# Kernel optimization log

Hardware: AMD Instinct MI355X
Metric: run time of the kernel (lower is better)

## Reference

```python
import jax, jax.numpy as jnp
import numpy as np
from jax import lax

EPS = 1e-6

def _instance_norm(x):
    # torch: std over flattened spatial, unbiased (ddof=1), + 1e-6
    b, c = x.shape[:2]
    xf = x.reshape(b, c, -1)
    mean = xf.mean(axis=2)[:, :, None, None]
    std = (jnp.std(xf, axis=2, ddof=1) + EPS)[:, :, None, None]
    return (x - mean) / std

def _conv1x1(x, w, b):
    # w: [O, I], x: [B, I, H, W]
    return jnp.einsum('oi,bihw->bohw', w, x) + b[None, :, None, None]

def _adaattn(content, style, ckey, skey, fw, fb, gw, gb, hw, hb):
    F = _conv1x1(ckey, fw, fb)   # [b, Ck, hc, wc]
    G = _conv1x1(skey, gw, gb)   # [b, Ck, hs, ws]
    H = _conv1x1(style, hw, hb)  # [b, Cv, hs, ws]
    b_, Ck, hc, wc = F.shape
    hs, ws = G.shape[2], G.shape[3]
    Fq = F.reshape(b_, Ck, hc * wc).transpose(0, 2, 1)   # [b, Nc, Ck]
    Gk = G.reshape(b_, Ck, hs * ws)                      # [b, Ck, Ns]
    Vs = H.reshape(b_, -1, hs * ws).transpose(0, 2, 1)   # [b, Ns, Cv]
    # Ns == hs*ws <= max_sample (4096) for these shapes -> no subsampling branch
    S = jax.nn.softmax(jnp.einsum('bnc,bcm->bnm', Fq, Gk), axis=-1)  # [b, Nc, Ns]
    mean = jnp.einsum('bnm,bmv->bnv', S, Vs)              # attention-weighted mean
    ex2 = jnp.einsum('bnm,bmv->bnv', S, Vs * Vs)          # E[x^2]
    std = jnp.sqrt(jax.nn.relu(ex2 - mean * mean))        # sqrt(relu(E[x^2]-E[x]^2))
    mean = mean.reshape(b_, hc, wc, -1).transpose(0, 3, 1, 2)
    std = std.reshape(b_, hc, wc, -1).transpose(0, 3, 1, 2)
    return std * _instance_norm(content) + mean

def _upsample2(x):
    return jnp.repeat(jnp.repeat(x, 2, axis=2), 2, axis=3)

def _conv3x3_reflect(x, w, b):
    xp = jnp.pad(x, ((0, 0), (0, 0), (1, 1), (1, 1)), mode='reflect')
    y = lax.conv_general_dilated(xp, w, window_strides=(1, 1), padding='VALID',
                                 dimension_numbers=('NCHW', 'OIHW', 'NCHW'))
    return y + b[None, :, None, None]


def setup_inputs() -> dict:
    key = jax.random.key(0)
    ks = jax.random.split(key, 16)
    f32 = jnp.float32
    d = {}
    d['content4_1'] = jax.random.normal(ks[0], (1, 512, 128, 128), f32)
    d['style4_1'] = jax.random.normal(ks[1], (1, 512, 64, 64), f32)
    d['content5_1'] = jax.random.normal(ks[2], (1, 512, 64, 64), f32)
    d['style5_1'] = jax.random.normal(ks[3], (1, 512, 32, 32), f32)
    d['content4_1_key'] = jax.random.normal(ks[4], (1, 960, 128, 128), f32)
    d['style4_1_key'] = jax.random.normal(ks[5], (1, 960, 64, 64), f32)
    d['content5_1_key'] = jax.random.normal(ks[6], (1, 1472, 64, 64), f32)
    d['style5_1_key'] = jax.random.normal(ks[7], (1, 1472, 32, 32), f32)
    def w2(k, o, i):
        return jax.random.normal(k, (o, i), f32) / np.sqrt(i).astype(np.float32)
    d['f4_w'] = w2(ks[8], 960, 960); d['f4_b'] = jnp.zeros((960,), f32)
    d['g4_w'] = w2(ks[9], 960, 960); d['g4_b'] = jnp.zeros((960,), f32)
    d['h4_w'] = w2(ks[10], 512, 512); d['h4_b'] = jnp.zeros((512,), f32)
    d['f5_w'] = w2(ks[11], 1472, 1472); d['f5_b'] = jnp.zeros((1472,), f32)
    d['g5_w'] = w2(ks[12], 1472, 1472); d['g5_b'] = jnp.zeros((1472,), f32)
    d['h5_w'] = w2(ks[13], 512, 512); d['h5_b'] = jnp.zeros((512,), f32)
    d['conv_w'] = jax.random.normal(ks[14], (512, 512, 3, 3), f32) / np.sqrt(512 * 9).astype(np.float32)
    d['conv_b'] = jnp.zeros((512,), f32)
    return d


def reference(content4_1, style4_1, content5_1, style5_1,
              content4_1_key, style4_1_key, content5_1_key, style5_1_key,
              f4_w, f4_b, g4_w, g4_b, h4_w, h4_b,
              f5_w, f5_b, g5_w, g5_b, h5_w, h5_b,
              conv_w, conv_b):
    a4 = _adaattn(content4_1, style4_1, content4_1_key, style4_1_key,
                  f4_w, f4_b, g4_w, g4_b, h4_w, h4_b)
    a5 = _adaattn(content5_1, style5_1, content5_1_key, style5_1_key,
                  f5_w, f5_b, g5_w, g5_b, h5_w, h5_b)
    return _conv3x3_reflect(a4 + _upsample2(a5), conv_w, conv_b)
```

## Files before the change

kernel.cpp:

```cpp
#include <hip/hip_runtime.h>
#include <math.h>


typedef _Float16 half8 __attribute__((ext_vector_type(8)));
typedef float f32x4 __attribute__((ext_vector_type(4)));

__device__ __forceinline__ void async16(const void* g, void* lds) {
    __builtin_amdgcn_global_load_lds(
        (const __attribute__((address_space(1))) void*)g,
        (__attribute__((address_space(3))) void*)lds, 16, 0, 0);
}

__device__ inline float wave_sum64(float v) {
#pragma unroll
    for (int o = 32; o > 0; o >>= 1) v += __shfl_xor(v, o, 64);
    return v;
}

template <int OUT>
__global__ __launch_bounds__(256, 2) void mgemm_hl(
    const _Float16* __restrict__ Ahi, const _Float16* __restrict__ Alo,
    const _Float16* __restrict__ Bhi, const _Float16* __restrict__ Blo,
    float* __restrict__ Cf, _Float16* __restrict__ Chi,
    _Float16* __restrict__ Clo, int K, int lda, int ldb, int ldc) {
    __shared__ _Float16 Ash[2][4096], Asl[2][4096], Bsh[2][4096], Bsl[2][4096];
    const int t = threadIdx.x, wave = t >> 6, lane = t & 63;
    const int bm = blockIdx.y * 128, bn = blockIdx.x * 128;
    const int wr = (wave >> 1) * 64, wc = (wave & 1) * 64;
    const int lq = lane >> 4, lr = lane & 15;
    const int srow = wave * 32 + (lane >> 2);
    const int scolg = (lane & 3) ^ ((lane >> 3) & 3);

    f32x4 acc[4][4] = {};

    const size_t aoff = (size_t)(bm + srow) * lda * 2 + scolg * 16;
    const size_t boff = (size_t)(bn + srow) * ldb * 2 + scolg * 16;
    const char* pAh = (const char*)Ahi + aoff;
    const char* pAl = (const char*)Alo + aoff;
    const char* pBh = (const char*)Bhi + boff;
    const char* pBl = (const char*)Blo + boff;
    const size_t ar = (size_t)16 * lda * 2, br = (size_t)16 * ldb * 2;
    const int dst = wave * 1024;
    const int key = (lr >> 1) & 3;

    auto stage = [&](int buf) {
        async16(pAh, &Ash[buf][dst]);
        async16(pAh + ar, &Ash[buf][dst + 512]);
        async16(pAl, &Asl[buf][dst]);
        async16(pAl + ar, &Asl[buf][dst + 512]);
        async16(pBh, &Bsh[buf][dst]);
        async16(pBh + br, &Bsh[buf][dst + 512]);
        async16(pBl, &Bsl[buf][dst]);
        async16(pBl + br, &Bsl[buf][dst + 512]);
        pAh += 64;
        pAl += 64;
        pBh += 64;
        pBl += 64;
    };

    const int NT = K >> 5;
    stage(0);
    for (int tt = 0; tt < NT; tt++) {
        __syncthreads();
        if (tt + 1 < NT) stage((tt + 1) & 1);
        const int cb = tt & 1;

        half8 ah[4], al[4], bh[4], bl[4];
#pragma unroll
        for (int i = 0; i < 4; i++) {
            const int ro = (wr + i * 16 + lr) * 32 + ((lq ^ key) * 8);
            ah[i] = *(const half8*)&Ash[cb][ro];
            al[i] = *(const half8*)&Asl[cb][ro];
        }
#pragma unroll
        for (int j = 0; j < 4; j++) {
            const int ro = (wc + j * 16 + lr) * 32 + ((lq ^ key) * 8);
            bh[j] = *(const half8*)&Bsh[cb][ro];
            bl[j] = *(const half8*)&Bsl[cb][ro];
        }
#pragma unroll
        for (int i = 0; i < 4; i++)
#pragma unroll
            for (int j = 0; j < 4; j++) {
                acc[i][j] = __builtin_amdgcn_mfma_f32_16x16x32_f16(
                    ah[i], bl[j], acc[i][j], 0, 0, 0);
                acc[i][j] = __builtin_amdgcn_mfma_f32_16x16x32_f16(
                    al[i], bh[j], acc[i][j], 0, 0, 0);
                acc[i][j] = __builtin_amdgcn_mfma_f32_16x16x32_f16(
                    ah[i], bh[j], acc[i][j], 0, 0, 0);
            }
    }
#pragma unroll
    for (int i = 0; i < 4; i++) {
        const int m0 = bm + wr + i * 16 + lq * 4;
#pragma unroll
        for (int j = 0; j < 4; j++) {
            const int n = bn + wc + j * 16 + lr;
#pragma unroll
            for (int r = 0; r < 4; r++) {
                const float v = acc[i][j][r];
                const size_t o = (size_t)(m0 + r) * ldc + n;
                if (OUT == 0) {
                    Cf[o] = v;
                } else {
                    _Float16 h = (_Float16)v;
                    Chi[o] = h;
                    Clo[o] = (_Float16)(v - (float)h);
                }
            }
        }
    }
}

template <int BIAS_MODE, int OUT_MODE, bool CONV>
__global__ __launch_bounds__(256, 2) void mgemm16(
    const _Float16* __restrict__ A, const _Float16* __restrict__ B,
    const float* __restrict__ bias, float* __restrict__ Cf,
    _Float16* __restrict__ Ch, int K, int lda, int ldb, int ldc,
    size_t splitStride) {
    __shared__ _Float16 As[2][4096];
    __shared__ _Float16 Bs[2][4096];
    const int t = threadIdx.x, wave = t >> 6, lane = t & 63;
    const int bm = blockIdx.y * 128, bn = blockIdx.x * 128;
    const int kbase = blockIdx.z * K;
    const int wr = (wave >> 1) * 64, wc = (wave & 1) * 64;
    const int lq = lane >> 4, lr = lane & 15;
    const int srow = wave * 32 + (lane >> 2);
    const int scolg = (lane & 3) ^ ((lane >> 3) & 3);

    f32x4 acc[4][4] = {};

    const char* Ap = (const char*)A +
                     ((size_t)(bm + srow) * lda + kbase) * 2 + scolg * 16;
    const char* Bp = (const char*)B +
                     ((size_t)(bn + srow) * ldb + kbase) * 2 + scolg * 16;
    const size_t Astep = (size_t)16 * lda * 2;
    const size_t Bstep = (size_t)16 * ldb * 2;
    const int dst = wave * 1024;
    const int key = (lr >> 1) & 3;

    auto stage = [&](int buf, int k0) {
        async16(Ap, &As[buf][dst]);
        async16(Ap + Astep, &As[buf][dst + 512]);
        Ap += 64;
        if (CONV) {
            const int kg = kbase + k0;
            const int rI = kg >> 9;
            const int dy = rI / 3, dx = rI - 3 * dy;
            const int ci0 = kg & 511;
            const char* Bc =
                (const char*)B +
                (((size_t)(blockIdx.x + dy) * 130 + srow + dx) * 512 + ci0) * 2 +
                scolg * 16;
            async16(Bc, &Bs[buf][dst]);
            async16(Bc + (size_t)16 * 512 * 2, &Bs[buf][dst + 512]);
        } else {
            async16(Bp, &Bs[buf][dst]);
            async16(Bp + Bstep, &Bs[buf][dst + 512]);
            Bp += 64;
        }
    };

    const int NT = K >> 5;
    stage(0, 0);
    for (int tt = 0; tt < NT; tt++) {
        __syncthreads();
        if (tt + 1 < NT) stage((tt + 1) & 1, (tt + 1) << 5);
        const int cb = tt & 1;

        half8 af[4], bf[4];
#pragma unroll
        for (int i = 0; i < 4; i++)
            af[i] =
                *(const half8*)&As[cb][(wr + i * 16 + lr) * 32 + (lq ^ key) * 8];
#pragma unroll
        for (int j = 0; j < 4; j++)
            bf[j] =
                *(const half8*)&Bs[cb][(wc + j * 16 + lr) * 32 + (lq ^ key) * 8];
#pragma unroll
        for (int i = 0; i < 4; i++)
#pragma unroll
            for (int j = 0; j < 4; j++)
                acc[i][j] = __builtin_amdgcn_mfma_f32_16x16x32_f16(
                    af[i], bf[j], acc[i][j], 0, 0, 0);
    }

    float* Co = (OUT_MODE == 0) ? Cf + (size_t)blockIdx.z * splitStride : nullptr;
#pragma unroll
    for (int i = 0; i < 4; i++) {
        const int m0 = bm + wr + i * 16 + lq * 4;
#pragma unroll
        for (int j = 0; j < 4; j++) {
            const int n = bn + wc + j * 16 + lr;
#pragma unroll
            for (int r = 0; r < 4; r++) {
                const int m = m0 + r;
                float v = acc[i][j][r];
                if (BIAS_MODE == 2) v += bias[m];
                if (OUT_MODE == 0) {
                    Co[(size_t)m * ldc + n] = v;
                } else {
                    Ch[(size_t)m * ldc + n] = (_Float16)v;
                    Ch[(size_t)(m + 512) * ldc + n] = (_Float16)(v * v);
                }
            }
        }
    }
}

__global__ __launch_bounds__(256) void transpose_hilo(
    const float* __restrict__ src, _Float16* __restrict__ dsthi,
    _Float16* __restrict__ dstlo, long srcld, int dstld, int nvalid,
    int cvalid) {
    __shared__ float tile[32][33];
    const int t = threadIdx.x, tx = t & 31, ty = t >> 5;
    const int n0 = blockIdx.x * 32, c0 = blockIdx.y * 32;
    const int n = n0 + tx;
#pragma unroll
    for (int i = 0; i < 4; i++) {
        int c = c0 + ty + i * 8;
        tile[ty + i * 8][tx] =
            (c < cvalid && n < nvalid) ? src[(size_t)c * srcld + n] : 0.f;
    }
    __syncthreads();
#pragma unroll
    for (int i = 0; i < 4; i++) {
        int nn = ty + i * 8;
        float v = tile[tx][nn];
        _Float16 h = (_Float16)v;
        size_t o = (size_t)(n0 + nn) * dstld + c0 + tx;
        dsthi[o] = h;
        dstlo[o] = (_Float16)(v - (float)h);
    }
}

__global__ __launch_bounds__(256) void transpose_cvt16(
    const float* __restrict__ src, _Float16* __restrict__ dst, long srcld,
    int dstld) {
    __shared__ float tile[32][33];
    const int t = threadIdx.x, tx = t & 31, ty = t >> 5;
    const int n0 = blockIdx.x * 32, c0 = blockIdx.y * 32;
#pragma unroll
    for (int i = 0; i < 4; i++)
        tile[ty + i * 8][tx] = src[(size_t)(c0 + ty + i * 8) * srcld + n0 + tx];
    __syncthreads();
#pragma unroll
    for (int i = 0; i < 4; i++) {
        int nn = ty + i * 8;
        dst[(size_t)(n0 + nn) * dstld + c0 + tx] = (_Float16)tile[tx][nn];
    }
}

__global__ __launch_bounds__(256) void cvt16(const float* __restrict__ src,
                                             _Float16* __restrict__ dst) {
    int i = blockIdx.x * 256 + threadIdx.x;
    dst[i] = (_Float16)src[i];
}

__global__ __launch_bounds__(256) void convw_perm(const float* __restrict__ src,
                                                  _Float16* __restrict__ dst) {
    int idx = blockIdx.x * 256 + threadIdx.x;
    int o = idx / 4608, rem = idx - o * 4608;
    int r = rem >> 9, ci = rem & 511;
    dst[idx] = (_Float16)src[(size_t)o * 4608 + ci * 9 + r];
}

__global__ __launch_bounds__(256) void fold_vec(
    const float* __restrict__ mat, const float* __restrict__ vec,
    const float* __restrict__ addc, float* __restrict__ outv, int C, int Nout,
    long ldm) {
    __shared__ float red[4][64];
    const int t = threadIdx.x, lane = t & 63, seg = t >> 6;
    const int n = blockIdx.x * 64 + lane;
    const int chunk = (C + 3) >> 2;
    const int start = seg * chunk;
    const int end = min(C, start + chunk);
    float s0 = 0.f, s1 = 0.f, s2 = 0.f, s3 = 0.f;
    if (n < Nout) {
        int c = start;
        for (; c + 3 < end; c += 4) {
            s0 = fmaf(vec[c], mat[(size_t)c * ldm + n], s0);
            s1 = fmaf(vec[c + 1], mat[(size_t)(c + 1) * ldm + n], s1);
            s2 = fmaf(vec[c + 2], mat[(size_t)(c + 2) * ldm + n], s2);
            s3 = fmaf(vec[c + 3], mat[(size_t)(c + 3) * ldm + n], s3);
        }
        for (; c < end; c++) s0 = fmaf(vec[c], mat[(size_t)c * ldm + n], s0);
    }
    red[seg][lane] = (s0 + s1) + (s2 + s3);
    __syncthreads();
    if (seg == 0 && n < Nout)
        outv[n] = red[0][lane] + red[1][lane] + red[2][lane] + red[3][lane] +
                  (addc ? addc[0] : 0.f);
}

__global__ __launch_bounds__(256) void dotbb(const float* __restrict__ a,
                                             const float* __restrict__ b,
                                             float* __restrict__ out, int C) {
    __shared__ float red[4];
    const int t = threadIdx.x;
    float s = 0.f;
    for (int c = t; c < C; c += 256) s = fmaf(a[c], b[c], s);
    s = wave_sum64(s);
    if ((t & 63) == 0) red[t >> 6] = s;
    __syncthreads();
    if (t == 0) out[0] = red[0] + red[1] + red[2] + red[3];
}

__global__ __launch_bounds__(256) void softmax_f16(
    const float* __restrict__ L, const float* __restrict__ rr,
    _Float16* __restrict__ S, int cols) {
    __shared__ float red_m[4], red_s[4];
    const int t = threadIdx.x;
    const float* p = L + (size_t)blockIdx.x * cols;
    _Float16* q = S + (size_t)blockIdx.x * cols;
    float mt = -3.0e38f, st = 0.f;
    for (int c = t; c < cols; c += 256) {
        float v = p[c] + rr[c];
        if (v > mt) {
            st = st * __expf(mt - v) + 1.f;
            mt = v;
        } else {
            st += __expf(v - mt);
        }
    }
#pragma unroll
    for (int o = 32; o > 0; o >>= 1) {
        float m2 = __shfl_xor(mt, o, 64), s2 = __shfl_xor(st, o, 64);
        float m = fmaxf(mt, m2);
        st = st * __expf(mt - m) + s2 * __expf(m2 - m);
        mt = m;
    }
    if ((t & 63) == 0) {
        red_m[t >> 6] = mt;
        red_s[t >> 6] = st;
    }
    __syncthreads();
    float M = fmaxf(fmaxf(red_m[0], red_m[1]), fmaxf(red_m[2], red_m[3]));
    float Ssum = red_s[0] * __expf(red_m[0] - M) +
                 red_s[1] * __expf(red_m[1] - M) +
                 red_s[2] * __expf(red_m[2] - M) +
                 red_s[3] * __expf(red_m[3] - M);
    float inv = 1.f / Ssum;
    for (int c = t; c < cols; c += 256)
        q[c] = (_Float16)(__expf(p[c] + rr[c] - M) * inv);
}

__global__ __launch_bounds__(256) void chanstats_kernel(
    const float* __restrict__ x, float* __restrict__ cm,
    float* __restrict__ cstd, int N) {
    __shared__ float rs[4], rs2[4];
    const int t = threadIdx.x;
    const float* p = x + (size_t)blockIdx.x * N;
    float s = 0.f, s2 = 0.f;
    for (int i = t; i < N; i += 256) {
        float v = p[i];
        s += v;
        s2 = fmaf(v, v, s2);
    }
    s = wave_sum64(s);
    s2 = wave_sum64(s2);
    if ((t & 63) == 0) {
        rs[t >> 6] = s;
        rs2[t >> 6] = s2;
    }
    __syncthreads();
    if (t == 0) {
        float S = rs[0] + rs[1] + rs[2] + rs[3];
        float S2 = rs2[0] + rs2[1] + rs2[2] + rs2[3];
        float mean = S / N;
        float var = fmaxf((S2 - S * mean) / (N - 1), 0.f);
        cm[blockIdx.x] = mean;
        cstd[blockIdx.x] = sqrtf(var) + 1e-6f;
    }
}

__global__ __launch_bounds__(256) void epilogue5(
    const float* __restrict__ pv, const float* __restrict__ content,
    const float* __restrict__ cm, const float* __restrict__ cstd,
    _Float16* __restrict__ a5t) {
    int idx = blockIdx.x * 256 + threadIdx.x;
    int n = idx >> 9, c = idx & 511;
    float mean = pv[(size_t)n * 1024 + c];
    float ex2 = pv[(size_t)n * 1024 + 512 + c];
    float sd = sqrtf(fmaxf(ex2 - mean * mean, 0.f));
    float cn = (content[(size_t)c * 4096 + n] - cm[c]) / cstd[c];
    a5t[idx] = (_Float16)(fmaf(sd, cn, mean));
}

__global__ __launch_bounds__(256) void epilogue4(
    const float* __restrict__ part, const float* __restrict__ content,
    const float* __restrict__ cm, const float* __restrict__ cstd,
    const _Float16* __restrict__ a5t, _Float16* __restrict__ pad4t, int n0) {
    int idx = blockIdx.x * 256 + threadIdx.x;
    int r = idx >> 9, c = idx & 511;
    int n = n0 + r;
    const size_t SS = (size_t)1024 * 1024;
    float mean = 0.f, ex2 = 0.f;
#pragma unroll
    for (int z = 0; z < 4; z++) {
        mean += part[z * SS + (size_t)r * 1024 + c];
        ex2 += part[z * SS + (size_t)r * 1024 + 512 + c];
    }
    float sd = sqrtf(fmaxf(ex2 - mean * mean, 0.f));
    float cn = (content[(size_t)c * 16384 + n] - cm[c]) / cstd[c];
    int y = n >> 7, x = n & 127;
    float up = (float)a5t[(size_t)((y >> 1) * 64 + (x >> 1)) * 512 + c];
    pad4t[(size_t)((y + 1) * 130 + (x + 1)) * 512 + c] =
        (_Float16)(fmaf(sd, cn, mean) + up);
}

__global__ __launch_bounds__(256) void border_kernel(_Float16* __restrict__ pad) {
    int idx = blockIdx.x * 256 + threadIdx.x;
    int pos = idx >> 9, c = idx & 511;
    int py, px;
    if (pos < 130) { py = 0; px = pos; }
    else if (pos < 260) { py = 129; px = pos - 130; }
    else if (pos < 388) { py = pos - 260 + 1; px = 0; }
    else { py = pos - 388 + 1; px = 129; }
    int sy = py == 0 ? 2 : (py == 129 ? 127 : py);
    int sx = px == 0 ? 2 : (px == 129 ? 127 : px);
    pad[(size_t)(py * 130 + px) * 512 + c] =
        pad[(size_t)(sy * 130 + sx) * 512 + c];
}


extern "C" void kernel_launch(void* const* d_in, const int* in_sizes, int n_in,
                              void* d_out, int out_size, void* d_ws,
                              size_t ws_size, hipStream_t stream) {
    (void)in_sizes; (void)n_in; (void)out_size; (void)ws_size;
    const float* content4 = (const float*)d_in[0];
    const float* style4 = (const float*)d_in[1];
    const float* content5 = (const float*)d_in[2];
    const float* style5 = (const float*)d_in[3];
    const float* ckey4 = (const float*)d_in[4];
    const float* skey4 = (const float*)d_in[5];
    const float* ckey5 = (const float*)d_in[6];
    const float* skey5 = (const float*)d_in[7];
    const float* f4w = (const float*)d_in[8];
    const float* f4b = (const float*)d_in[9];
    const float* g4w = (const float*)d_in[10];
    const float* g4b = (const float*)d_in[11];
    const float* h4w = (const float*)d_in[12];
    const float* h4b = (const float*)d_in[13];
    const float* f5w = (const float*)d_in[14];
    const float* f5b = (const float*)d_in[15];
    const float* g5w = (const float*)d_in[16];
    const float* g5b = (const float*)d_in[17];
    const float* h5w = (const float*)d_in[18];
    const float* h5b = (const float*)d_in[19];
    const float* convw = (const float*)d_in[20];
    const float* convb = (const float*)d_in[21];
    float* out = (float*)d_out;
    char* ws = (char*)d_ws;

    _Float16* PAD4T = (_Float16*)(ws + 0);
    _Float16* A5T = (_Float16*)(ws + 17305600);
    float* STATS = (float*)(ws + 21499904);
    _Float16* H4W = (_Float16*)(ws + 21508096);
    _Float16* H5W = (_Float16*)(ws + 22032384);
    _Float16* CONVW = (_Float16*)(ws + 22556672);
    float* U5 = (float*)(ws + 27275264);
    float* R5 = (float*)(ws + 27283456);
    float* U4 = (float*)(ws + 27291648);
    float* R4 = (float*)(ws + 27299840);
    float* BB5 = (float*)(ws + 27316224);
    float* BB4 = (float*)(ws + 27316480);
    char* A0 = ws + 27320320;

    float* cm4 = STATS, *cstd4 = STATS + 512, *cm5 = STATS + 1024,
         *cstd5 = STATS + 1536;

    chanstats_kernel<<<512, 256, 0, stream>>>(content5, cm5, cstd5, 4096);
    chanstats_kernel<<<512, 256, 0, stream>>>(content4, cm4, cstd4, 16384);
    cvt16<<<1024, 256, 0, stream>>>(h4w, H4W);
    cvt16<<<1024, 256, 0, stream>>>(h5w, H5W);
    convw_perm<<<9216, 256, 0, stream>>>(convw, CONVW);

    {
        _Float16* M5h = (_Float16*)(A0 + 0);
        _Float16* M5l = (_Float16*)(A0 + 4718592);
        _Float16* FWh = (_Float16*)(A0 + 9437184);
        _Float16* FWl = (_Float16*)(A0 + 14155776);
        _Float16* GWh = (_Float16*)(A0 + 18874368);
        _Float16* GWl = (_Float16*)(A0 + 23592960);
        _Float16* SKh = (_Float16*)(A0 + 9437184);
        _Float16* SKl = (_Float16*)(A0 + 12582912);
        _Float16* T5h = (_Float16*)(A0 + 15728640);
        _Float16* T5l = (_Float16*)(A0 + 18874368);
        _Float16* STT5 = (_Float16*)(A0 + 0);
        _Float16* HCAT5 = (_Float16*)(A0 + 1048576);
        _Float16* CKh = (_Float16*)(A0 + 22020096);
        _Float16* CKl = (_Float16*)(A0 + 34603008);
        float* LOG5 = (float*)(A0 + 47185920);
        _Float16* S5 = (_Float16*)(A0 + 63963136);

        dotbb<<<1, 256, 0, stream>>>(f5b, g5b, BB5, 1472);
        fold_vec<<<23, 256, 0, stream>>>(g5w, f5b, nullptr, U5, 1472, 1472, 1472);
        fold_vec<<<16, 256, 0, stream>>>(skey5, U5, BB5, R5, 1472, 1024, 1024);

        transpose_hilo<<<dim3(48, 48), 256, 0, stream>>>(f5w, FWh, FWl, 1472,
                                                         1536, 1472, 1472);
        transpose_hilo<<<dim3(48, 48), 256, 0, stream>>>(g5w, GWh, GWl, 1472,
                                                         1536, 1472, 1472);
        mgemm_hl<1><<<dim3(12, 12), 256, 0, stream>>>(
            FWh, FWl, GWh, GWl, nullptr, M5h, M5l, 1536, 1536, 1536, 1536);
        transpose_hilo<<<dim3(32, 48), 256, 0, stream>>>(skey5, SKh, SKl, 1024,
                                                         1536, 1024, 1472);
        mgemm_hl<1><<<dim3(12, 8), 256, 0, stream>>>(
            SKh, SKl, M5h, M5l, nullptr, T5h, T5l, 1536, 1536, 1536, 1536);
        transpose_cvt16<<<dim3(32, 16), 256, 0, stream>>>(style5, STT5, 1024, 512);
        mgemm16<2, 2, false><<<dim3(8, 4), 256, 0, stream>>>(
            H5W, STT5, h5b, nullptr, HCAT5, 512, 512, 512, 1024, 0);
        transpose_hilo<<<dim3(128, 48), 256, 0, stream>>>(ckey5, CKh, CKl, 4096,
                                                          1536, 4096, 1472);
        mgemm_hl<0><<<dim3(8, 32), 256, 0, stream>>>(
            CKh, CKl, T5h, T5l, LOG5, nullptr, nullptr, 1536, 1536, 1536, 1024);
        softmax_f16<<<4096, 256, 0, stream>>>(LOG5, R5, S5, 1024);
        mgemm16<0, 0, false><<<dim3(8, 32), 256, 0, stream>>>(
            S5, HCAT5, nullptr, LOG5 , nullptr, 1024, 1024, 1024, 1024,
            (size_t)4096 * 1024);
        epilogue5<<<8192, 256, 0, stream>>>(LOG5, content5, cm5, cstd5, A5T);
    }

    {
        _Float16* T4h = (_Float16*)(A0 + 0);
        _Float16* T4l = (_Float16*)(A0 + 8388608);
        _Float16* M4h = (_Float16*)(A0 + 16777216);
        _Float16* M4l = (_Float16*)(A0 + 18874368);
        _Float16* FWh = (_Float16*)(A0 + 20971520);
        _Float16* FWl = (_Float16*)(A0 + 23068672);
        _Float16* GWh = (_Float16*)(A0 + 25165824);
        _Float16* GWl = (_Float16*)(A0 + 27262976);
        _Float16* SKh = (_Float16*)(A0 + 29360128);
        _Float16* SKl = (_Float16*)(A0 + 37748736);
        _Float16* STT4 = (_Float16*)(A0 + 16777216);
        _Float16* HCAT4 = (_Float16*)(A0 + 20971520);
        _Float16* CKh = (_Float16*)(A0 + 29360128);
        _Float16* CKl = (_Float16*)(A0 + 31457280);
        _Float16* S4 = (_Float16*)(A0 + 33554432);
        float* LOGR = (float*)(A0 + 41943040);

        dotbb<<<1, 256, 0, stream>>>(f4b, g4b, BB4, 960);
        fold_vec<<<15, 256, 0, stream>>>(g4w, f4b, nullptr, U4, 960, 960, 960);
        fold_vec<<<64, 256, 0, stream>>>(skey4, U4, BB4, R4, 960, 4096, 4096);

        transpose_hilo<<<dim3(32, 32), 256, 0, stream>>>(f4w, FWh, FWl, 960,
                                                         1024, 960, 960);
        transpose_hilo<<<dim3(32, 32), 256, 0, stream>>>(g4w, GWh, GWl, 960,
                                                         1024, 960, 960);
        mgemm_hl<1><<<dim3(8, 8), 256, 0, stream>>>(
            FWh, FWl, GWh, GWl, nullptr, M4h, M4l, 1024, 1024, 1024, 1024);
        transpose_hilo<<<dim3(128, 32), 256, 0, stream>>>(skey4, SKh, SKl, 4096,
                                                          1024, 4096, 960);
        mgemm_hl<1><<<dim3(8, 32), 256, 0, stream>>>(
            SKh, SKl, M4h, M4l, nullptr, T4h, T4l, 1024, 1024, 1024, 1024);
        transpose_cvt16<<<dim3(128, 16), 256, 0, stream>>>(style4, STT4, 4096, 512);
        mgemm16<2, 2, false><<<dim3(32, 4), 256, 0, stream>>>(
            H4W, STT4, h4b, nullptr, HCAT4, 512, 512, 512, 4096, 0);

        for (int chunk = 0; chunk < 16; chunk++) {
            const int n0 = chunk * 1024;
            transpose_hilo<<<dim3(32, 32), 256, 0, stream>>>(
                ckey4 + n0, CKh, CKl, 16384, 1024, 1024, 960);
            mgemm_hl<0><<<dim3(32, 8), 256, 0, stream>>>(
                CKh, CKl, T4h, T4l, LOGR, nullptr, nullptr, 1024, 1024, 1024,
                4096);
            softmax_f16<<<1024, 256, 0, stream>>>(LOGR, R4, S4, 4096);
            mgemm16<0, 0, false><<<dim3(8, 8, 4), 256, 0, stream>>>(
                S4, HCAT4, nullptr, LOGR , nullptr, 1024, 4096, 4096,
                1024, (size_t)1024 * 1024);
            epilogue4<<<2048, 256, 0, stream>>>(LOGR, content4, cm4, cstd4, A5T,
                                                PAD4T, n0);
        }
    }

    border_kernel<<<1032, 256, 0, stream>>>(PAD4T);
    mgemm16<2, 0, true><<<dim3(128, 4), 256, 0, stream>>>(
        CONVW, PAD4T, convb, out, nullptr, 4608, 4608, 512, 16384, 0);
}
```

Measured before the change: 2.413 ms.

## Deepen GEMM LDS pipelines with vmcnt waits and vectorize register-resident softmax

Moves both MFMA GEMM kernels from double-buffered LDS staging with __syncthreads to deeper buffering: triple for the hi/lo kernel, quadruple for the fp16 kernel. Each iteration waits with explicit s_waitcnt vmcnt counts before the barrier, so global-to-LDS loads can stay in flight across more k-steps. The softmax is rewritten to hold each row in registers with float4 loads, do separate max and sum reductions, and write half4 stores, reading the logits once instead of twice. The larger LDS footprint (96KB and 64KB per block) may limit the two-blocks-per-CU occupancy the launch bounds request. The hand-counted vmcnt values rely on each stage issuing exactly 8 or 4 loads.

```diff
diff --git a/kernel.cpp b/kernel.cpp
--- a/kernel.cpp
+++ b/kernel.cpp
@@ -3,7 +3,10 @@
 
 
 typedef _Float16 half8 __attribute__((ext_vector_type(8)));
+typedef _Float16 half4 __attribute__((ext_vector_type(4)));
 typedef float f32x4 __attribute__((ext_vector_type(4)));
+
+#define VMCNT(n) asm volatile("s_waitcnt vmcnt(" #n ")" ::: "memory")
 
 __device__ __forceinline__ void async16(const void* g, void* lds) {
     __builtin_amdgcn_global_load_lds(
@@ -23,7 +26,7 @@
     const _Float16* __restrict__ Bhi, const _Float16* __restrict__ Blo,
     float* __restrict__ Cf, _Float16* __restrict__ Chi,
     _Float16* __restrict__ Clo, int K, int lda, int ldb, int ldc) {
-    __shared__ _Float16 Ash[2][4096], Asl[2][4096], Bsh[2][4096], Bsl[2][4096];
+    __shared__ _Float16 Ash[3][4096], Asl[3][4096], Bsh[3][4096], Bsl[3][4096];
     const int t = threadIdx.x, wave = t >> 6, lane = t & 63;
     const int bm = blockIdx.y * 128, bn = blockIdx.x * 128;
     const int wr = (wave >> 1) * 64, wc = (wave & 1) * 64;
@@ -60,10 +63,19 @@
 
     const int NT = K >> 5;
     stage(0);
+    if (NT > 1) stage(1);
     for (int tt = 0; tt < NT; tt++) {
-        __syncthreads();
-        if (tt + 1 < NT) stage((tt + 1) & 1);
-        const int cb = tt & 1;
+        if (tt + 1 < NT) {
+            VMCNT(8);
+        } else {
+            VMCNT(0);
+        }
+        __builtin_amdgcn_s_barrier();
+        {
+            const int nx = tt + 2;
+            if (nx < NT) stage(nx % 3);
+        }
+        const int cb = tt % 3;
 
         half8 ah[4], al[4], bh[4], bl[4];
 #pragma unroll
@@ -118,8 +130,8 @@
     const float* __restrict__ bias, float* __restrict__ Cf,
     _Float16* __restrict__ Ch, int K, int lda, int ldb, int ldc,
     size_t splitStride) {
-    __shared__ _Float16 As[2][4096];
-    __shared__ _Float16 Bs[2][4096];
+    __shared__ _Float16 As[4][4096];
+    __shared__ _Float16 Bs[4][4096];
     const int t = threadIdx.x, wave = t >> 6, lane = t & 63;
     const int bm = blockIdx.y * 128, bn = blockIdx.x * 128;
     const int kbase = blockIdx.z * K;
@@ -163,10 +175,19 @@
 
     const int NT = K >> 5;
     stage(0, 0);
+    if (NT > 1) stage(1, 32);
+    if (NT > 2) stage(2, 64);
     for (int tt = 0; tt < NT; tt++) {
-        __syncthreads();
-        if (tt + 1 < NT) stage((tt + 1) & 1, (tt + 1) << 5);
-        const int cb = tt & 1;
+        if (tt + 2 < NT) {
+            VMCNT(8);
+        } else if (tt + 1 < NT) {
+            VMCNT(4);
+        } else {
+            VMCNT(0);
+        }
+        __builtin_amdgcn_s_barrier();
+        if (tt + 3 < NT) stage((tt + 3) & 3, (tt + 3) << 5);
+        const int cb = tt & 3;
 
         half8 af[4], bf[4];
 #pragma unroll
@@ -306,43 +327,54 @@
     if (t == 0) out[0] = red[0] + red[1] + red[2] + red[3];
 }
 
-__global__ __launch_bounds__(256) void softmax_f16(
-    const float* __restrict__ L, const float* __restrict__ rr,
-    _Float16* __restrict__ S, int cols) {
-    __shared__ float red_m[4], red_s[4];
+template <int NPER>
+__global__ __launch_bounds__(256) void softmax2(const float* __restrict__ L,
+                                                const float* __restrict__ rr,
+                                                _Float16* __restrict__ S) {
+    constexpr int NV = NPER / 4;
+    __shared__ float redm[4], reds[4];
     const int t = threadIdx.x;
-    const float* p = L + (size_t)blockIdx.x * cols;
-    _Float16* q = S + (size_t)blockIdx.x * cols;
-    float mt = -3.0e38f, st = 0.f;
-    for (int c = t; c < cols; c += 256) {
-        float v = p[c] + rr[c];
-        if (v > mt) {
-            st = st * __expf(mt - v) + 1.f;
-            mt = v;
-        } else {
-            st += __expf(v - mt);
-        }
-    }
-#pragma unroll
-    for (int o = 32; o > 0; o >>= 1) {
-        float m2 = __shfl_xor(mt, o, 64), s2 = __shfl_xor(st, o, 64);
-        float m = fmaxf(mt, m2);
-        st = st * __expf(mt - m) + s2 * __expf(m2 - m);
-        mt = m;
-    }
-    if ((t & 63) == 0) {
-        red_m[t >> 6] = mt;
-        red_s[t >> 6] = st;
-    }
+    const float* p = L + (size_t)blockIdx.x * (NPER * 256);
+    _Float16* q = S + (size_t)blockIdx.x * (NPER * 256);
+    f32x4 v[NV];
+    float m = -3.0e38f;
+#pragma unroll
+    for (int i = 0; i < NV; i++) {
+        const int c = t * 4 + i * 1024;
+        f32x4 x = *(const f32x4*)(p + c);
+        const f32x4 r = *(const f32x4*)(rr + c);
+        x = x + r;
+        v[i] = x;
+        m = fmaxf(m, fmaxf(fmaxf(x[0], x[1]), fmaxf(x[2], x[3])));
+    }
+#pragma unroll
+    for (int o = 32; o > 0; o >>= 1) m = fmaxf(m, __shfl_xor(m, o, 64));
+    if ((t & 63) == 0) redm[t >> 6] = m;
     __syncthreads();
-    float M = fmaxf(fmaxf(red_m[0], red_m[1]), fmaxf(red_m[2], red_m[3]));
-    float Ssum = red_s[0] * __expf(red_m[0] - M) +
-                 red_s[1] * __expf(red_m[1] - M) +
-                 red_s[2] * __expf(red_m[2] - M) +
-                 red_s[3] * __expf(red_m[3] - M);
-    float inv = 1.f / Ssum;
-    for (int c = t; c < cols; c += 256)
-        q[c] = (_Float16)(__expf(p[c] + rr[c] - M) * inv);
+    m = fmaxf(fmaxf(redm[0], redm[1]), fmaxf(redm[2], redm[3]));
+    float s = 0.f;
+#pragma unroll
+    for (int i = 0; i < NV; i++) {
+        f32x4 x = v[i];
+#pragma unroll
+        for (int j = 0; j < 4; j++) {
+            x[j] = __expf(x[j] - m);
+            s += x[j];
+        }
+        v[i] = x;
+    }
+    s = wave_sum64(s);
+    if ((t & 63) == 0) reds[t >> 6] = s;
+    __syncthreads();
+    const float inv = 1.f / (reds[0] + reds[1] + reds[2] + reds[3]);
+#pragma unroll
+    for (int i = 0; i < NV; i++) {
+        const int c = t * 4 + i * 1024;
+        half4 h;
+#pragma unroll
+        for (int j = 0; j < 4; j++) h[j] = (_Float16)(v[i][j] * inv);
+        *(half4*)(q + c) = h;
+    }
 }
 
 __global__ __launch_bounds__(256) void chanstats_kernel(
@@ -515,7 +547,7 @@
                                                           1536, 4096, 1472);
         mgemm_hl<0><<<dim3(8, 32), 256, 0, stream>>>(
             CKh, CKl, T5h, T5l, LOG5, nullptr, nullptr, 1536, 1536, 1536, 1024);
-        softmax_f16<<<4096, 256, 0, stream>>>(LOG5, R5, S5, 1024);
+        softmax2<4><<<4096, 256, 0, stream>>>(LOG5, R5, S5);
         mgemm16<0, 0, false><<<dim3(8, 32), 256, 0, stream>>>(
             S5, HCAT5, nullptr, LOG5 , nullptr, 1024, 1024, 1024, 1024,
             (size_t)4096 * 1024);
@@ -565,7 +597,7 @@
             mgemm_hl<0><<<dim3(32, 8), 256, 0, stream>>>(
                 CKh, CKl, T4h, T4l, LOGR, nullptr, nullptr, 1024, 1024, 1024,
                 4096);
-            softmax_f16<<<1024, 256, 0, stream>>>(LOGR, R4, S4, 4096);
+            softmax2<16><<<1024, 256, 0, stream>>>(LOGR, R4, S4);
             mgemm16<0, 0, false><<<dim3(8, 8, 4), 256, 0, stream>>>(
                 S4, HCAT4, nullptr, LOGR , nullptr, 1024, 4096, 4096,
                 1024, (size_t)1024 * 1024);
```

New measurement: 2.338 ms. -3.1%, faster.
